# Kernel tuning notes

Hardware: AMD Instinct MI355X
Metric: run time of the kernel (lower is better)

Reference implementation:

```python
import jax, jax.numpy as jnp
import numpy as np

B, S, D, H = 1, 2048, 1024, 16
DH = D // H  # 64
ROPE_THETA = 10000.0


def _rope_tables(seq_len, half_dim, theta):
    inv = 1.0 / (theta ** (np.arange(0, half_dim, dtype=np.float32) / half_dim))
    ang = np.arange(seq_len, dtype=np.float32)[:, None] * inv[None, :]
    return jnp.asarray(np.cos(ang)), jnp.asarray(np.sin(ang))


def setup_inputs() -> dict:
    key = jax.random.key(0)
    ks = jax.random.split(key, 6)
    x = jax.random.normal(ks[0], (B, S, D), dtype=jnp.float32)
    # block-diagonal mask over ~4 packed images -> sorted segment ids
    seg_ids = jnp.sort(jax.random.randint(ks[1], (S,), 0, 4, dtype=jnp.int32))
    freqs_cos, freqs_sin = _rope_tables(S, DH // 2, ROPE_THETA)
    scale = 1.0 / np.sqrt(D)
    wq = jax.random.normal(ks[2], (D, D), dtype=jnp.float32) * scale
    wk = jax.random.normal(ks[3], (D, D), dtype=jnp.float32) * scale
    wv = jax.random.normal(ks[4], (D, D), dtype=jnp.float32) * scale
    wo = jax.random.normal(ks[5], (D, D), dtype=jnp.float32) * scale
    return {"x": x, "seg_ids": seg_ids, "freqs_cos": freqs_cos,
            "freqs_sin": freqs_sin, "wq": wq, "wk": wk, "wv": wv, "wo": wo}


def _apply_rope(t, cos, sin):
    # t: [B,S,H,DH]; interpret last dim as DH//2 complex pairs (real, imag)
    tr = t.reshape(B, S, H, DH // 2, 2)
    a, b = tr[..., 0], tr[..., 1]
    c = cos[None, :, None, :]  # [1,S,1,DH/2]
    s = sin[None, :, None, :]
    out = jnp.stack([a * c - b * s, a * s + b * c], axis=-1)
    return out.reshape(B, S, H, DH)


def reference(x, seg_ids, freqs_cos, freqs_sin, wq, wk, wv, wo):
    q = (x @ wq.T).reshape(B, S, H, DH)
    k = (x @ wk.T).reshape(B, S, H, DH)
    v = (x @ wv.T).reshape(B, S, H, DH)
    q = _apply_rope(q, freqs_cos, freqs_sin)
    k = _apply_rope(k, freqs_cos, freqs_sin)
    scores = jnp.einsum('bqhd,bkhd->bhqk', q, k) / np.float32(np.sqrt(DH))
    block_mask = (seg_ids[:, None] == seg_ids[None, :])  # [S,S] block-diagonal
    scores = jnp.where(block_mask[None, None], scores, jnp.float32(-1e9))
    attn = jax.nn.softmax(scores, axis=-1)
    out = jnp.einsum('bhqk,bkhd->bqhd', attn, v).reshape(B, S, D)
    return out @ wo.T
```

## Files before the change

kernel.cpp:

```cpp
#include <hip/hip_runtime.h>

typedef __bf16 bf16;
typedef __bf16 bf16x4 __attribute__((ext_vector_type(4)));
typedef __bf16 bf16x8 __attribute__((ext_vector_type(8)));
typedef float  f32x4  __attribute__((ext_vector_type(4)));

#define S_LEN 2048
#define D_DIM 1024
#define NHEAD 16
#define DHEAD 64
#define NPAR 4

__device__ __forceinline__ void async_cp16(const bf16* g, bf16* l) {
  __builtin_amdgcn_global_load_lds(
      (__attribute__((address_space(1))) void*)(void*)g,
      (__attribute__((address_space(3))) void*)l,
      16, 0, 0);
}

__global__ __launch_bounds__(256) void cvt_k(
    const float* __restrict__ x,  const float* __restrict__ w0,
    const float* __restrict__ w1, const float* __restrict__ w2,
    const float* __restrict__ w3, bf16* __restrict__ dst,
    const int* __restrict__ seg, int* __restrict__ kbr)
{
  __shared__ int firstv[4];
  const int b = blockIdx.x;
  const int t = threadIdx.x;

  if (b < 3072) {
    int i = b * 256 + t;
    const float* src;
    int off;
    if (i < (1 << 18)) {
      src = x; off = i;
    } else {
      int j = i - (1 << 18);
      int s = j >> 17;
      off = j & ((1 << 17) - 1);
      src = (s == 0) ? w0 : (s == 1) ? w1 : (s == 2) ? w2 : w3;
    }
    f32x4 a = *(const f32x4*)(src + (size_t)off * 8);
    f32x4 bb = *(const f32x4*)(src + (size_t)off * 8 + 4);
    bf16x8 o;
    o[0] = (bf16)a[0];  o[1] = (bf16)a[1];  o[2] = (bf16)a[2];  o[3] = (bf16)a[3];
    o[4] = (bf16)bb[0]; o[5] = (bf16)bb[1]; o[6] = (bf16)bb[2]; o[7] = (bf16)bb[3];
    *((bf16x8*)dst + i) = o;
  } else {
    if (t < 4) firstv[t] = S_LEN;
    __syncthreads();
    for (int i = t; i < S_LEN; i += 256) {
      int s = seg[i];
      if (i == 0 || seg[i - 1] != s) atomicMin(&firstv[s], i);
    }
    __syncthreads();
    if (t < 32) {
      int smin = seg[t * 64], smax = seg[t * 64 + 63];
      int lb = S_LEN, ub = S_LEN;
      for (int vv = smin; vv < 4; ++vv) lb = min(lb, firstv[vv]);
      for (int vv = smax + 1; vv < 4; ++vv) ub = min(ub, firstv[vv]);
      kbr[t * 2] = lb >> 6;
      kbr[t * 2 + 1] = (ub - 1) >> 6;
    }
  }
}

__global__ __launch_bounds__(256) void gemm_qkv(
    const bf16* __restrict__ A,
    const bf16* __restrict__ B0, const bf16* __restrict__ B1,
    const bf16* __restrict__ B2,
    const float* __restrict__ cosT, const float* __restrict__ sinT,
    bf16* __restrict__ Cbase, bf16* __restrict__ Vt)
{
  constexpr int K = 1024, N = 1024;
  const int z = blockIdx.z;
  const bf16* W = (z == 0) ? B0 : (z == 1) ? B1 : B2;
  bf16* C = Cbase + (size_t)z * 2048 * 1024;

  __shared__ bf16 As[4][128 * 32] __attribute__((aligned(16)));
  __shared__ bf16 Bs[4][64 * 32] __attribute__((aligned(16)));

  const int t = threadIdx.x;
  const int lane = t & 63;
  const int w = t >> 6;
  const int lm = lane & 15, lq = lane >> 4;
  const int wr = w >> 1, wc = w & 1;
  const int bm = blockIdx.y, bn = blockIdx.x;

  const bf16* Abase = A + (size_t)bm * 128 * K;
  const bf16* Wbase = W + (size_t)bn * 64 * K;

  f32x4 acc[4][2] = {};

  for (int kk = 0; kk < K; kk += 128) {
#pragma unroll
    for (int kh = 0; kh < 2; ++kh)
#pragma unroll
      for (int g = 0; g < 2; ++g) {
        int c = (w * 2 + g) * 64 + lane;
        int row = c >> 2, k8 = c & 3;
        const bf16* ga = Abase + (size_t)row * K + kk + kh * 64 + k8 * 8;
        async_cp16(ga, &As[kh * 2][(w * 2 + g) * 512]);
        async_cp16(ga + 32, &As[kh * 2 + 1][(w * 2 + g) * 512]);
      }
#pragma unroll
    for (int kh = 0; kh < 2; ++kh) {
      int c = w * 64 + lane;
      int row = c >> 2, k8 = c & 3;
      const bf16* gb = Wbase + (size_t)row * K + kk + kh * 64 + k8 * 8;
      async_cp16(gb, &Bs[kh * 2][w * 512]);
      async_cp16(gb + 32, &Bs[kh * 2 + 1][w * 512]);
    }
    __syncthreads();

#pragma unroll
    for (int ks = 0; ks < 4; ++ks) {
      bf16x8 af[4], bfr[2];
#pragma unroll
      for (int mi = 0; mi < 4; ++mi)
        af[mi] = *(const bf16x8*)&As[ks][(wr * 64 + mi * 16 + lm) * 32 + lq * 8];
#pragma unroll
      for (int ni = 0; ni < 2; ++ni)
        bfr[ni] = *(const bf16x8*)&Bs[ks][(wc * 32 + ni * 16 + lm) * 32 + lq * 8];
#pragma unroll
      for (int mi = 0; mi < 4; ++mi)
#pragma unroll
        for (int ni = 0; ni < 2; ++ni)
          acc[mi][ni] = __builtin_amdgcn_mfma_f32_16x16x32_bf16(
              af[mi], bfr[ni], acc[mi][ni], 0, 0, 0);
    }
    __syncthreads();
  }

  if (z < 2) {
    const float scale = (z == 0) ? 0.125f : 1.0f;
#pragma unroll
    for (int mi = 0; mi < 4; ++mi)
#pragma unroll
      for (int ni = 0; ni < 2; ++ni) {
        int gcol = bn * 64 + wc * 32 + ni * 16 + lm;
        int p = (gcol & 63) >> 1;
        bool even = (gcol & 1) == 0;
#pragma unroll
        for (int r = 0; r < 4; ++r) {
          int row = bm * 128 + wr * 64 + mi * 16 + lq * 4 + r;
          float v = acc[mi][ni][r];
          float mate = __shfl_xor(v, 1);
          float cv = cosT[row * 32 + p];
          float sv = sinT[row * 32 + p];
          float res = even ? (v * cv - mate * sv) : (mate * sv + v * cv);
          C[(size_t)row * N + gcol] = (bf16)(res * scale);
        }
      }
  } else {
#pragma unroll
    for (int mi = 0; mi < 4; ++mi)
#pragma unroll
      for (int ni = 0; ni < 2; ++ni) {
        int gcol = bn * 64 + wc * 32 + ni * 16 + lm;
        int rowb = bm * 128 + wr * 64 + mi * 16 + lq * 4;
        bf16x4 pack;
#pragma unroll
        for (int r = 0; r < 4; ++r) pack[r] = (bf16)acc[mi][ni][r];
        *(bf16x4*)(Vt + (size_t)gcol * S_LEN + rowb) = pack;
      }
  }
}

__global__ __launch_bounds__(256) void gemm_wo(
    const bf16* __restrict__ A, const bf16* __restrict__ W,
    float* __restrict__ C)
{
  constexpr int K = 1024, N = 1024;

  __shared__ bf16 As[4][64 * 32] __attribute__((aligned(16)));
  __shared__ bf16 Bs[4][64 * 32] __attribute__((aligned(16)));

  const int t = threadIdx.x;
  const int lane = t & 63;
  const int w = t >> 6;
  const int lm = lane & 15, lq = lane >> 4;
  const int bn = blockIdx.x, bm = blockIdx.y;

  const bf16* Abase = A + (size_t)bm * 64 * K;
  const bf16* Wbase = W + (size_t)bn * 64 * K;

  f32x4 acc[4] = {};

  for (int kk = 0; kk < K; kk += 128) {
#pragma unroll
    for (int kh = 0; kh < 2; ++kh) {
      int c = w * 64 + lane;
      int row = c >> 2, k8 = c & 3;
      const bf16* ga = Abase + (size_t)row * K + kk + kh * 64 + k8 * 8;
      async_cp16(ga, &As[kh * 2][w * 512]);
      async_cp16(ga + 32, &As[kh * 2 + 1][w * 512]);
      const bf16* gb = Wbase + (size_t)row * K + kk + kh * 64 + k8 * 8;
      async_cp16(gb, &Bs[kh * 2][w * 512]);
      async_cp16(gb + 32, &Bs[kh * 2 + 1][w * 512]);
    }
    __syncthreads();

#pragma unroll
    for (int ks = 0; ks < 4; ++ks) {
      bf16x8 af = *(const bf16x8*)&As[ks][(w * 16 + lm) * 32 + lq * 8];
      bf16x8 bfr[4];
#pragma unroll
      for (int ni = 0; ni < 4; ++ni)
        bfr[ni] = *(const bf16x8*)&Bs[ks][(ni * 16 + lm) * 32 + lq * 8];
#pragma unroll
      for (int ni = 0; ni < 4; ++ni)
        acc[ni] = __builtin_amdgcn_mfma_f32_16x16x32_bf16(
            af, bfr[ni], acc[ni], 0, 0, 0);
    }
    __syncthreads();
  }

#pragma unroll
  for (int ni = 0; ni < 4; ++ni) {
    int col = bn * 64 + ni * 16 + lm;
#pragma unroll
    for (int r = 0; r < 4; ++r) {
      int row = bm * 64 + w * 16 + lq * 4 + r;
      C[(size_t)row * N + col] = acc[ni][r];
    }
  }
}

__global__ __launch_bounds__(256) void attn_k(
    const bf16* __restrict__ Q, const bf16* __restrict__ Kmat,
    const bf16* __restrict__ Vt, const int* __restrict__ seg,
    const int* __restrict__ kbr,
    float* __restrict__ Opar, float* __restrict__ Lpar)
{
  __shared__ bf16 Ks[64 * 72] __attribute__((aligned(16)));
  __shared__ bf16 Vs[64 * 72] __attribute__((aligned(16)));
  __shared__ bf16 Ps[4][16 * 72] __attribute__((aligned(16)));
  __shared__ int segk[64];

  const int h = blockIdx.y;
  const int qt = blockIdx.x & 31, par = blockIdx.x >> 5;
  const int q0 = qt * 64;
  const int t = threadIdx.x, lane = t & 63, w = t >> 6;
  const int lm = lane & 15, lq = lane >> 4;
  const int qrow = q0 + w * 16;

  const int kb0f = kbr[qt * 2], kb1f = kbr[qt * 2 + 1];

  bf16x8 qf[2];
#pragma unroll
  for (int ks = 0; ks < 2; ++ks)
    qf[ks] = *(const bf16x8*)(Q + (size_t)(qrow + lm) * D_DIM + h * DHEAD +
                              ks * 32 + lq * 8);

  int sq[4];
  float l_i[4];
#pragma unroll
  for (int r = 0; r < 4; ++r) {
    sq[r] = seg[qrow + lq * 4 + r];
    l_i[r] = 0.0f;
  }
  f32x4 o[4] = {};

  const int srow0 = t >> 3, sch = (t & 7) * 8;
  const int srow1 = (256 + t) >> 3;

  const int kbS = kb0f + par;
  f32x4 pk0, pk1, pv0, pv1;
  int psg;
  if (kbS <= kb1f) {
    const int k0 = kbS * 64;
    pk0 = *(const f32x4*)(Kmat + (size_t)(k0 + srow0) * D_DIM + h * DHEAD + sch);
    pk1 = *(const f32x4*)(Kmat + (size_t)(k0 + srow1) * D_DIM + h * DHEAD + sch);
    pv0 = *(const f32x4*)(Vt + (size_t)(h * DHEAD + srow0) * S_LEN + k0 + sch);
    pv1 = *(const f32x4*)(Vt + (size_t)(h * DHEAD + srow1) * S_LEN + k0 + sch);
    if (t < 64) psg = seg[k0 + t];
  }

  for (int kb = kbS; kb <= kb1f; kb += NPAR) {
    __syncthreads();
    *(f32x4*)&Ks[srow0 * 72 + sch] = pk0;
    *(f32x4*)&Ks[srow1 * 72 + sch] = pk1;
    *(f32x4*)&Vs[srow0 * 72 + sch] = pv0;
    *(f32x4*)&Vs[srow1 * 72 + sch] = pv1;
    if (t < 64) segk[t] = psg;
    __syncthreads();

    if (kb + NPAR <= kb1f) {
      const int k0 = (kb + NPAR) * 64;
      pk0 = *(const f32x4*)(Kmat + (size_t)(k0 + srow0) * D_DIM + h * DHEAD + sch);
      pk1 = *(const f32x4*)(Kmat + (size_t)(k0 + srow1) * D_DIM + h * DHEAD + sch);
      pv0 = *(const f32x4*)(Vt + (size_t)(h * DHEAD + srow0) * S_LEN + k0 + sch);
      pv1 = *(const f32x4*)(Vt + (size_t)(h * DHEAD + srow1) * S_LEN + k0 + sch);
      if (t < 64) psg = seg[k0 + t];
    }

    f32x4 sa[4] = {};
#pragma unroll
    for (int ks = 0; ks < 2; ++ks) {
      bf16x8 kf[4];
#pragma unroll
      for (int ni = 0; ni < 4; ++ni)
        kf[ni] = *(const bf16x8*)&Ks[(ni * 16 + lm) * 72 + ks * 32 + lq * 8];
#pragma unroll
      for (int ni = 0; ni < 4; ++ni)
        sa[ni] = __builtin_amdgcn_mfma_f32_16x16x32_bf16(qf[ks], kf[ni],
                                                         sa[ni], 0, 0, 0);
    }

    int sk[4];
#pragma unroll
    for (int ni = 0; ni < 4; ++ni) sk[ni] = segk[ni * 16 + lm];

#pragma unroll
    for (int r = 0; r < 4; ++r)
#pragma unroll
      for (int ni = 0; ni < 4; ++ni) {
        float p = (sq[r] == sk[ni]) ? __expf(sa[ni][r]) : 0.0f;
        l_i[r] += p;
        Ps[w][(lq * 4 + r) * 72 + ni * 16 + lm] = (bf16)p;
      }

#pragma unroll
    for (int ks = 0; ks < 2; ++ks) {
      bf16x8 pf = *(const bf16x8*)&Ps[w][lm * 72 + ks * 32 + lq * 8];
      bf16x8 vf[4];
#pragma unroll
      for (int ni = 0; ni < 4; ++ni)
        vf[ni] = *(const bf16x8*)&Vs[(ni * 16 + lm) * 72 + ks * 32 + lq * 8];
#pragma unroll
      for (int ni = 0; ni < 4; ++ni)
        o[ni] = __builtin_amdgcn_mfma_f32_16x16x32_bf16(pf, vf[ni], o[ni],
                                                        0, 0, 0);
    }
  }

  float* Ob = Opar + ((size_t)(par * NHEAD + h) * S_LEN) * DHEAD;
  float* Lb = Lpar + (size_t)(par * NHEAD + h) * S_LEN;
#pragma unroll
  for (int r = 0; r < 4; ++r) {
    float l = l_i[r];
    l += __shfl_xor(l, 1);
    l += __shfl_xor(l, 2);
    l += __shfl_xor(l, 4);
    l += __shfl_xor(l, 8);
    int row = qrow + lq * 4 + r;
    if (lm == 0) Lb[row] = l;
#pragma unroll
    for (int ni = 0; ni < 4; ++ni)
      Ob[(size_t)row * DHEAD + ni * 16 + lm] = o[ni][r];
  }
}

__global__ __launch_bounds__(256) void combine_k(
    const float* __restrict__ Opar, const float* __restrict__ Lpar,
    bf16* __restrict__ AO)
{
  int idx = blockIdx.x * 256 + threadIdx.x;
  int c4 = idx & 15;
  int rh = idx >> 4;
  int row = rh & 2047;
  int h = rh >> 11;
  const size_t PO = (size_t)NHEAD * S_LEN * DHEAD;
  const size_t PL = (size_t)NHEAD * S_LEN;
  const float* o0 = Opar + ((size_t)h * S_LEN + row) * DHEAD + c4 * 4;
  f32x4 s = {0.f, 0.f, 0.f, 0.f};
  float l = 0.f;
#pragma unroll
  for (int p = 0; p < NPAR; ++p) {
    s += *(const f32x4*)(o0 + p * PO);
    l += Lpar[p * PL + (size_t)h * S_LEN + row];
  }
  float inv = 1.0f / l;
  bf16x4 ov;
#pragma unroll
  for (int j = 0; j < 4; ++j) ov[j] = (bf16)(s[j] * inv);
  *(bf16x4*)(AO + (size_t)row * D_DIM + h * DHEAD + c4 * 4) = ov;
}

extern "C" void kernel_launch(void* const* d_in, const int* in_sizes, int n_in,
                              void* d_out, int out_size, void* d_ws,
                              size_t ws_size, hipStream_t stream)
{
  const float* x  = (const float*)d_in[0];
  const int*   sg = (const int*)d_in[1];
  const float* fc = (const float*)d_in[2];
  const float* fs = (const float*)d_in[3];
  const float* wq = (const float*)d_in[4];
  const float* wk = (const float*)d_in[5];
  const float* wv = (const float*)d_in[6];
  const float* wo = (const float*)d_in[7];
  float* out = (float*)d_out;

  const size_t MAT = (size_t)S_LEN * D_DIM;
  const size_t WSZ = (size_t)D_DIM * D_DIM;
  bf16* xb  = (bf16*)d_ws;
  bf16* wqb = xb + MAT;
  bf16* wkb = wqb + WSZ;
  bf16* wvb = wkb + WSZ;
  bf16* wob = wvb + WSZ;
  bf16* q0  = wob + WSZ;
  bf16* k0  = q0 + MAT;
  bf16* vt  = k0 + MAT;
  bf16* ao  = vt + MAT;
  float* opar = (float*)(ao + MAT);
  float* lpar = opar + (size_t)NPAR * MAT;
  int*   kbr  = (int*)(lpar + (size_t)NPAR * NHEAD * S_LEN);

  dim3 blk(256);
  cvt_k<<<dim3(3073), blk, 0, stream>>>(x, wq, wk, wv, wo, xb, sg, kbr);
  gemm_qkv<<<dim3(16, 16, 3), blk, 0, stream>>>(xb, wqb, wkb, wvb, fc, fs,
                                                q0, vt);
  attn_k<<<dim3(32 * NPAR, 16), blk, 0, stream>>>(q0, k0, vt, sg, kbr,
                                                  opar, lpar);
  combine_k<<<dim3(2048), blk, 0, stream>>>(opar, lpar, ao);
  gemm_wo<<<dim3(16, 32), blk, 0, stream>>>(ao, wob, out);
}
```

Baseline: 147.3 us.

## Double attention query tile to 128 rows per block to reuse K/V tiles

```diff
diff --git a/kernel.cpp b/kernel.cpp
--- a/kernel.cpp
+++ b/kernel.cpp
@@ -54,8 +54,8 @@
       if (i == 0 || seg[i - 1] != s) atomicMin(&firstv[s], i);
     }
     __syncthreads();
-    if (t < 32) {
-      int smin = seg[t * 64], smax = seg[t * 64 + 63];
+    if (t < 16) {
+      int smin = seg[t * 128], smax = seg[t * 128 + 127];
       int lb = S_LEN, ub = S_LEN;
       for (int vv = smin; vv < 4; ++vv) lb = min(lb, firstv[vv]);
       for (int vv = smax + 1; vv < 4; ++vv) ub = min(ub, firstv[vv]);
@@ -235,32 +235,36 @@
 {
   __shared__ bf16 Ks[64 * 72] __attribute__((aligned(16)));
   __shared__ bf16 Vs[64 * 72] __attribute__((aligned(16)));
-  __shared__ bf16 Ps[4][16 * 72] __attribute__((aligned(16)));
+  __shared__ bf16 Ps[4][32 * 72] __attribute__((aligned(16)));
   __shared__ int segk[64];
 
   const int h = blockIdx.y;
-  const int qt = blockIdx.x & 31, par = blockIdx.x >> 5;
-  const int q0 = qt * 64;
+  const int qt = blockIdx.x & 15, par = blockIdx.x >> 4;
+  const int q0 = qt * 128;
   const int t = threadIdx.x, lane = t & 63, w = t >> 6;
   const int lm = lane & 15, lq = lane >> 4;
-  const int qrow = q0 + w * 16;
 
   const int kb0f = kbr[qt * 2], kb1f = kbr[qt * 2 + 1];
 
-  bf16x8 qf[2];
-#pragma unroll
-  for (int ks = 0; ks < 2; ++ks)
-    qf[ks] = *(const bf16x8*)(Q + (size_t)(qrow + lm) * D_DIM + h * DHEAD +
-                              ks * 32 + lq * 8);
-
-  int sq[4];
-  float l_i[4];
-#pragma unroll
-  for (int r = 0; r < 4; ++r) {
-    sq[r] = seg[qrow + lq * 4 + r];
-    l_i[r] = 0.0f;
-  }
-  f32x4 o[4] = {};
+  bf16x8 qf[2][2];
+#pragma unroll
+  for (int mf = 0; mf < 2; ++mf)
+#pragma unroll
+    for (int ks = 0; ks < 2; ++ks)
+      qf[mf][ks] = *(const bf16x8*)(Q +
+          (size_t)(q0 + w * 16 + mf * 64 + lm) * D_DIM + h * DHEAD +
+          ks * 32 + lq * 8);
+
+  int sq[2][4];
+  float l_i[2][4];
+#pragma unroll
+  for (int mf = 0; mf < 2; ++mf)
+#pragma unroll
+    for (int r = 0; r < 4; ++r) {
+      sq[mf][r] = seg[q0 + w * 16 + mf * 64 + lq * 4 + r];
+      l_i[mf][r] = 0.0f;
+    }
+  f32x4 o[2][4] = {};
 
   const int srow0 = t >> 3, sch = (t & 7) * 8;
   const int srow1 = (256 + t) >> 3;
@@ -295,7 +299,7 @@
       if (t < 64) psg = seg[k0 + t];
     }
 
-    f32x4 sa[4] = {};
+    f32x4 sa[2][4] = {};
 #pragma unroll
     for (int ks = 0; ks < 2; ++ks) {
       bf16x8 kf[4];
@@ -303,9 +307,11 @@
       for (int ni = 0; ni < 4; ++ni)
         kf[ni] = *(const bf16x8*)&Ks[(ni * 16 + lm) * 72 + ks * 32 + lq * 8];
 #pragma unroll
-      for (int ni = 0; ni < 4; ++ni)
-        sa[ni] = __builtin_amdgcn_mfma_f32_16x16x32_bf16(qf[ks], kf[ni],
-                                                         sa[ni], 0, 0, 0);
+      for (int mf = 0; mf < 2; ++mf)
+#pragma unroll
+        for (int ni = 0; ni < 4; ++ni)
+          sa[mf][ni] = __builtin_amdgcn_mfma_f32_16x16x32_bf16(
+              qf[mf][ks], kf[ni], sa[mf][ni], 0, 0, 0);
     }
 
     int sk[4];
@@ -313,43 +319,51 @@
     for (int ni = 0; ni < 4; ++ni) sk[ni] = segk[ni * 16 + lm];
 
 #pragma unroll
-    for (int r = 0; r < 4; ++r)
-#pragma unroll
-      for (int ni = 0; ni < 4; ++ni) {
-        float p = (sq[r] == sk[ni]) ? __expf(sa[ni][r]) : 0.0f;
-        l_i[r] += p;
-        Ps[w][(lq * 4 + r) * 72 + ni * 16 + lm] = (bf16)p;
-      }
+    for (int mf = 0; mf < 2; ++mf)
+#pragma unroll
+      for (int r = 0; r < 4; ++r)
+#pragma unroll
+        for (int ni = 0; ni < 4; ++ni) {
+          float p = (sq[mf][r] == sk[ni]) ? __expf(sa[mf][ni][r]) : 0.0f;
+          l_i[mf][r] += p;
+          Ps[w][(mf * 16 + lq * 4 + r) * 72 + ni * 16 + lm] = (bf16)p;
+        }
 
 #pragma unroll
     for (int ks = 0; ks < 2; ++ks) {
-      bf16x8 pf = *(const bf16x8*)&Ps[w][lm * 72 + ks * 32 + lq * 8];
       bf16x8 vf[4];
 #pragma unroll
       for (int ni = 0; ni < 4; ++ni)
         vf[ni] = *(const bf16x8*)&Vs[(ni * 16 + lm) * 72 + ks * 32 + lq * 8];
 #pragma unroll
-      for (int ni = 0; ni < 4; ++ni)
-        o[ni] = __builtin_amdgcn_mfma_f32_16x16x32_bf16(pf, vf[ni], o[ni],
-                                                        0, 0, 0);
+      for (int mf = 0; mf < 2; ++mf) {
+        bf16x8 pf = *(const bf16x8*)&Ps[w][(mf * 16 + lm) * 72 +
+                                           ks * 32 + lq * 8];
+#pragma unroll
+        for (int ni = 0; ni < 4; ++ni)
+          o[mf][ni] = __builtin_amdgcn_mfma_f32_16x16x32_bf16(
+              pf, vf[ni], o[mf][ni], 0, 0, 0);
+      }
     }
   }
 
   float* Ob = Opar + ((size_t)(par * NHEAD + h) * S_LEN) * DHEAD;
   float* Lb = Lpar + (size_t)(par * NHEAD + h) * S_LEN;
 #pragma unroll
-  for (int r = 0; r < 4; ++r) {
-    float l = l_i[r];
-    l += __shfl_xor(l, 1);
-    l += __shfl_xor(l, 2);
-    l += __shfl_xor(l, 4);
-    l += __shfl_xor(l, 8);
-    int row = qrow + lq * 4 + r;
-    if (lm == 0) Lb[row] = l;
-#pragma unroll
-    for (int ni = 0; ni < 4; ++ni)
-      Ob[(size_t)row * DHEAD + ni * 16 + lm] = o[ni][r];
-  }
+  for (int mf = 0; mf < 2; ++mf)
+#pragma unroll
+    for (int r = 0; r < 4; ++r) {
+      float l = l_i[mf][r];
+      l += __shfl_xor(l, 1);
+      l += __shfl_xor(l, 2);
+      l += __shfl_xor(l, 4);
+      l += __shfl_xor(l, 8);
+      int row = q0 + w * 16 + mf * 64 + lq * 4 + r;
+      if (lm == 0) Lb[row] = l;
+#pragma unroll
+      for (int ni = 0; ni < 4; ++ni)
+        Ob[(size_t)row * DHEAD + ni * 16 + lm] = o[mf][ni][r];
+    }
 }
 
 __global__ __launch_bounds__(256) void combine_k(
@@ -411,7 +425,7 @@
   cvt_k<<<dim3(3073), blk, 0, stream>>>(x, wq, wk, wv, wo, xb, sg, kbr);
   gemm_qkv<<<dim3(16, 16, 3), blk, 0, stream>>>(xb, wqb, wkb, wvb, fc, fs,
                                                 q0, vt);
-  attn_k<<<dim3(32 * NPAR, 16), blk, 0, stream>>>(q0, k0, vt, sg, kbr,
+  attn_k<<<dim3(16 * NPAR, 16), blk, 0, stream>>>(q0, k0, vt, sg, kbr,
                                                   opar, lpar);
   combine_k<<<dim3(2048), blk, 0, stream>>>(opar, lpar, ao);
   gemm_wo<<<dim3(16, 32), blk, 0, stream>>>(ao, wob, out);
```

Result: slower. 150.6 us (+2.3%).

## Double-buffer LDS tiles in QKV and output-projection GEMMs

Applied to the files above, without the earlier changes.

```diff
diff --git a/kernel.cpp b/kernel.cpp
--- a/kernel.cpp
+++ b/kernel.cpp
@@ -77,8 +77,8 @@
   const bf16* W = (z == 0) ? B0 : (z == 1) ? B1 : B2;
   bf16* C = Cbase + (size_t)z * 2048 * 1024;
 
-  __shared__ bf16 As[4][128 * 32] __attribute__((aligned(16)));
-  __shared__ bf16 Bs[4][64 * 32] __attribute__((aligned(16)));
+  __shared__ bf16 As[2][2][128 * 32] __attribute__((aligned(16)));
+  __shared__ bf16 Bs[2][2][64 * 32] __attribute__((aligned(16)));
 
   const int t = threadIdx.x;
   const int lane = t & 63;
@@ -92,36 +92,40 @@
 
   f32x4 acc[4][2] = {};
 
-  for (int kk = 0; kk < K; kk += 128) {
-#pragma unroll
-    for (int kh = 0; kh < 2; ++kh)
-#pragma unroll
-      for (int g = 0; g < 2; ++g) {
-        int c = (w * 2 + g) * 64 + lane;
-        int row = c >> 2, k8 = c & 3;
-        const bf16* ga = Abase + (size_t)row * K + kk + kh * 64 + k8 * 8;
-        async_cp16(ga, &As[kh * 2][(w * 2 + g) * 512]);
-        async_cp16(ga + 32, &As[kh * 2 + 1][(w * 2 + g) * 512]);
-      }
-#pragma unroll
-    for (int kh = 0; kh < 2; ++kh) {
+  auto stage = [&](int kk, int buf) {
+#pragma unroll
+    for (int g = 0; g < 2; ++g) {
+      int c = (w * 2 + g) * 64 + lane;
+      int row = c >> 2, k8 = c & 3;
+      const bf16* ga = Abase + (size_t)row * K + kk + k8 * 8;
+      async_cp16(ga, &As[buf][0][(w * 2 + g) * 512]);
+      async_cp16(ga + 32, &As[buf][1][(w * 2 + g) * 512]);
+    }
+    {
       int c = w * 64 + lane;
       int row = c >> 2, k8 = c & 3;
-      const bf16* gb = Wbase + (size_t)row * K + kk + kh * 64 + k8 * 8;
-      async_cp16(gb, &Bs[kh * 2][w * 512]);
-      async_cp16(gb + 32, &Bs[kh * 2 + 1][w * 512]);
-    }
-    __syncthreads();
-
-#pragma unroll
-    for (int ks = 0; ks < 4; ++ks) {
+      const bf16* gb = Wbase + (size_t)row * K + kk + k8 * 8;
+      async_cp16(gb, &Bs[buf][0][w * 512]);
+      async_cp16(gb + 32, &Bs[buf][1][w * 512]);
+    }
+  };
+
+  stage(0, 0);
+  for (int it = 0; it < 16; ++it) {
+    const int buf = it & 1;
+    __syncthreads();
+    if (it < 15) stage((it + 1) * 64, buf ^ 1);
+#pragma unroll
+    for (int ks = 0; ks < 2; ++ks) {
       bf16x8 af[4], bfr[2];
 #pragma unroll
       for (int mi = 0; mi < 4; ++mi)
-        af[mi] = *(const bf16x8*)&As[ks][(wr * 64 + mi * 16 + lm) * 32 + lq * 8];
+        af[mi] = *(const bf16x8*)&As[buf][ks][(wr * 64 + mi * 16 + lm) * 32 +
+                                             lq * 8];
 #pragma unroll
       for (int ni = 0; ni < 2; ++ni)
-        bfr[ni] = *(const bf16x8*)&Bs[ks][(wc * 32 + ni * 16 + lm) * 32 + lq * 8];
+        bfr[ni] = *(const bf16x8*)&Bs[buf][ks][(wc * 32 + ni * 16 + lm) * 32 +
+                                               lq * 8];
 #pragma unroll
       for (int mi = 0; mi < 4; ++mi)
 #pragma unroll
@@ -129,7 +133,6 @@
           acc[mi][ni] = __builtin_amdgcn_mfma_f32_16x16x32_bf16(
               af[mi], bfr[ni], acc[mi][ni], 0, 0, 0);
     }
-    __syncthreads();
   }
 
   if (z < 2) {
@@ -173,8 +176,8 @@
 {
   constexpr int K = 1024, N = 1024;
 
-  __shared__ bf16 As[4][64 * 32] __attribute__((aligned(16)));
-  __shared__ bf16 Bs[4][64 * 32] __attribute__((aligned(16)));
+  __shared__ bf16 As[2][4][64 * 32] __attribute__((aligned(16)));
+  __shared__ bf16 Bs[2][4][64 * 32] __attribute__((aligned(16)));
 
   const int t = threadIdx.x;
   const int lane = t & 63;
@@ -187,33 +190,37 @@
 
   f32x4 acc[4] = {};
 
-  for (int kk = 0; kk < K; kk += 128) {
+  auto stage = [&](int kk, int buf) {
 #pragma unroll
     for (int kh = 0; kh < 2; ++kh) {
       int c = w * 64 + lane;
       int row = c >> 2, k8 = c & 3;
       const bf16* ga = Abase + (size_t)row * K + kk + kh * 64 + k8 * 8;
-      async_cp16(ga, &As[kh * 2][w * 512]);
-      async_cp16(ga + 32, &As[kh * 2 + 1][w * 512]);
+      async_cp16(ga, &As[buf][kh * 2][w * 512]);
+      async_cp16(ga + 32, &As[buf][kh * 2 + 1][w * 512]);
       const bf16* gb = Wbase + (size_t)row * K + kk + kh * 64 + k8 * 8;
-      async_cp16(gb, &Bs[kh * 2][w * 512]);
-      async_cp16(gb + 32, &Bs[kh * 2 + 1][w * 512]);
-    }
-    __syncthreads();
-
+      async_cp16(gb, &Bs[buf][kh * 2][w * 512]);
+      async_cp16(gb + 32, &Bs[buf][kh * 2 + 1][w * 512]);
+    }
+  };
+
+  stage(0, 0);
+  for (int it = 0; it < 8; ++it) {
+    const int buf = it & 1;
+    __syncthreads();
+    if (it < 7) stage((it + 1) * 128, buf ^ 1);
 #pragma unroll
     for (int ks = 0; ks < 4; ++ks) {
-      bf16x8 af = *(const bf16x8*)&As[ks][(w * 16 + lm) * 32 + lq * 8];
+      bf16x8 af = *(const bf16x8*)&As[buf][ks][(w * 16 + lm) * 32 + lq * 8];
       bf16x8 bfr[4];
 #pragma unroll
       for (int ni = 0; ni < 4; ++ni)
-        bfr[ni] = *(const bf16x8*)&Bs[ks][(ni * 16 + lm) * 32 + lq * 8];
+        bfr[ni] = *(const bf16x8*)&Bs[buf][ks][(ni * 16 + lm) * 32 + lq * 8];
 #pragma unroll
       for (int ni = 0; ni < 4; ++ni)
         acc[ni] = __builtin_amdgcn_mfma_f32_16x16x32_bf16(
             af, bfr[ni], acc[ni], 0, 0, 0);
     }
-    __syncthreads();
   }
 
 #pragma unroll
```

Result: no change. 149.6 us (+1.6%).
